# Optimization experiments

Measured on AMD Instinct MI355X. Metric: run time of the kernel, lower is better.

Reference implementation:

```python
import jax, jax.numpy as jnp
import numpy as np
from jax import lax

GAMMA = 0.99
LAM = 0.95
CLIP_PARAM = 0.2
VALUE_LOSS_COEF = 0.5
ENTROPY_COEF = 0.01
EPS = 1e-09

B, T = 4096, 2048


def setup_inputs() -> dict:
    key = jax.random.key(0)
    ks = jax.random.split(key, 6)
    rewards = jax.random.normal(ks[0], (B, T), dtype=jnp.float32)
    values = jax.random.normal(ks[1], (B, T + 1), dtype=jnp.float32)
    ref_probs = jax.random.uniform(ks[2], (B, T), dtype=jnp.float32)
    old_probs = jax.random.uniform(ks[3], (B, T), dtype=jnp.float32)
    curr_probs = jax.random.uniform(ks[4], (B, T), dtype=jnp.float32)
    # episode-continuation masks: mostly 1, occasional 0 (episode boundary)
    masks = (jax.random.uniform(ks[5], (B, T)) > 0.02).astype(jnp.float32)
    return {"rewards": rewards, "values": values, "ref_probs": ref_probs,
            "old_probs": old_probs, "curr_probs": curr_probs, "masks": masks}


def compute_gae(rewards, values, masks, gamma, lam):
    # single fused reverse scan over time; per-step state is (B,)
    def step(carry, xs):
        r, v, v_next, m = xs
        delta = r + gamma * v_next * m - v
        adv = delta + gamma * lam * m * carry
        return adv, adv

    xs = (rewards.T, values[:, :-1].T, values[:, 1:].T, masks.T)  # each (T, B)
    _, advs = lax.scan(step, jnp.zeros(rewards.shape[0], rewards.dtype), xs, reverse=True)
    advantages = advs.T  # (B, T)
    returns = advantages + values[:, :-1]
    return advantages, returns


def reference(rewards, values, ref_probs, old_probs, curr_probs, masks):
    advantages, returns = compute_gae(rewards, values, masks, GAMMA, LAM)
    # torch .std() is unbiased (ddof=1)
    advantages = (advantages - advantages.mean()) / (advantages.std(ddof=1) + EPS)
    ratios = curr_probs / (old_probs + EPS)
    surr1 = ratios * advantages
    surr2 = jnp.clip(ratios, 1.0 - CLIP_PARAM, 1.0 + CLIP_PARAM) * advantages
    ppo_loss = -jnp.minimum(surr1, surr2).mean()
    value_loss = jnp.mean((returns - values[:, :-1]) ** 2)
    entropy_loss = -jnp.mean(curr_probs * jnp.log(curr_probs + EPS))
    total_loss = ppo_loss + VALUE_LOSS_COEF * value_loss + ENTROPY_COEF * entropy_loss
    return (total_loss, ppo_loss, VALUE_LOSS_COEF * value_loss, ENTROPY_COEF * entropy_loss)
```

## Files before the change

kernel.cpp:

```cpp
#include <hip/hip_runtime.h>
#include <math.h>


#define GAMMA     0.99f
#define LAM       0.95f
#define CLIP_LO   0.8f
#define CLIP_HI   1.2f
#define EPSF      1e-9f

constexpr int BB = 4096;
constexpr int TT = 2048;
constexpr long long NN = (long long)BB * TT;
constexpr int GAE_BLOCKS = BB;
constexpr int PPO_BLOCKS = 4096;

struct Stats { float mean; float inv; double sum2; };
static constexpr size_t GAE_PART_OFF = 64;
static constexpr size_t PPO_PART_OFF = GAE_PART_OFF + GAE_BLOCKS * sizeof(float2);
static constexpr size_t ADV_OFF      = PPO_PART_OFF + PPO_BLOCKS * sizeof(float2);

__device__ __forceinline__ unsigned bf16_rne(float x) {
    unsigned u = __float_as_uint(x);
    u += 0x7FFFu + ((u >> 16) & 1u);
    return u >> 16;
}

__global__ __launch_bounds__(512, 4) void gae_kernel(
    const float* __restrict__ rewards,
    const float* __restrict__ values,
    const float* __restrict__ masks,
    uint4* __restrict__ advb,
    float2* __restrict__ partials)
{
    const int tid  = threadIdx.x;
    const int lane = tid & 63;
    const int wave = tid >> 6;
    const int e0   = tid * 4;
    const int r    = blockIdx.x;

    __shared__ float2 wT[8];
    __shared__ float  wr1[8], wr2[8];

    const float* rp = rewards + (size_t)r * TT;
    const float* mp = masks   + (size_t)r * TT;
    const size_t vw  = (size_t)r * (TT + 1);
    const int    ofs = (int)(vw & 3);
    const float4* v4 = (const float4*)(values + (vw & ~(size_t)3));

    float4 R  = *(const float4*)(rp + e0);
    float4 M  = *(const float4*)(mp + e0);
    float4 V0 = v4[tid];
    float4 V1 = v4[tid + 1];

    float ff[8] = {V0.x, V0.y, V0.z, V0.w, V1.x, V1.y, V1.z, V1.w};
    float vv[5];
    if (ofs == 0) {
#pragma unroll
        for (int j = 0; j < 5; ++j) vv[j] = ff[j];
    } else if (ofs == 1) {
#pragma unroll
        for (int j = 0; j < 5; ++j) vv[j] = ff[j + 1];
    } else if (ofs == 2) {
#pragma unroll
        for (int j = 0; j < 5; ++j) vv[j] = ff[j + 2];
    } else {
#pragma unroll
        for (int j = 0; j < 5; ++j) vv[j] = ff[j + 3];
    }

    float rr[4] = {R.x, R.y, R.z, R.w};
    float mm[4] = {M.x, M.y, M.z, M.w};

    float la[4], S[4];
    {
        float d[4], c[4];
#pragma unroll
        for (int j = 0; j < 4; ++j) {
            d[j] = rr[j] + GAMMA * vv[j + 1] * mm[j] - vv[j];
            c[j] = (GAMMA * LAM) * mm[j];
        }
        la[3] = d[3]; S[3] = c[3];
#pragma unroll
        for (int j = 2; j >= 0; --j) {
            la[j] = d[j] + c[j] * la[j + 1];
            S[j]  = c[j] * S[j + 1];
        }
    }

    float A = S[0], Bv = la[0];
#pragma unroll
    for (int d2 = 1; d2 < 64; d2 <<= 1) {
        float A2 = __shfl_down(A, d2, 64), B2 = __shfl_down(Bv, d2, 64);
        if (lane + d2 < 64) { Bv = Bv + A * B2; A = A * A2; }
    }
    if (lane == 0) wT[wave] = make_float2(A, Bv);
    __syncthreads();
    float C = 0.f;
    for (int ww = 7; ww > wave; --ww) C = wT[ww].y + wT[ww].x * C;
    float A1 = __shfl_down(A, 1, 64), B1 = __shfl_down(Bv, 1, 64);
    float car = (lane < 63) ? (B1 + A1 * C) : C;

    float s1 = 0.f, s2 = 0.f;
    unsigned hh[4];
#pragma unroll
    for (int j = 0; j < 4; ++j) {
        float a = la[j] + S[j] * car;
        s1 += a; s2 += a * a;
        hh[j] = bf16_rne(a);
    }
    uint2 pk = {hh[0] | (hh[1] << 16), hh[2] | (hh[3] << 16)};
    ((uint2*)advb)[(size_t)r * 512 + tid] = pk;

#pragma unroll
    for (int off = 32; off > 0; off >>= 1) {
        s1 += __shfl_down(s1, off, 64);
        s2 += __shfl_down(s2, off, 64);
    }
    if (lane == 0) { wr1[wave] = s1; wr2[wave] = s2; }
    __syncthreads();
    if (tid == 0) {
        float t1 = 0.f, t2 = 0.f;
#pragma unroll
        for (int w = 0; w < 8; ++w) { t1 += wr1[w]; t2 += wr2[w]; }
        partials[blockIdx.x] = make_float2(t1, t2);
    }
}

__global__ __launch_bounds__(256) void finalize_stats(
    const float2* __restrict__ gp, Stats* __restrict__ stats)
{
    const int tid = threadIdx.x;
    __shared__ double l1[256], l2[256];
    double s1 = 0.0, s2 = 0.0;
    for (int i = tid; i < GAE_BLOCKS; i += 256) {
        float2 p = gp[i];
        s1 += (double)p.x;
        s2 += (double)p.y;
    }
    l1[tid] = s1; l2[tid] = s2;
    __syncthreads();
    for (int st = 128; st > 0; st >>= 1) {
        if (tid < st) { l1[tid] += l1[tid + st]; l2[tid] += l2[tid + st]; }
        __syncthreads();
    }
    if (tid == 0) {
        double S1 = l1[0], S2 = l2[0];
        double mean = S1 / (double)NN;
        double var  = (S2 - S1 * S1 / (double)NN) / (double)(NN - 1);
        stats->mean = (float)mean;
        stats->inv  = (float)(1.0 / (sqrt(var) + 1e-9));
        stats->sum2 = S2;
    }
}

__global__ __launch_bounds__(256, 8) void ppo_kernel(
    const float* __restrict__ adv_bf16,
    const float* __restrict__ oldp,
    const float* __restrict__ currp,
    const Stats* __restrict__ stats,
    float2* __restrict__ partials)
{
    const float mean = stats->mean;
    const float inv  = stats->inv;
    const int tid = threadIdx.x;
    const int i0  = blockIdx.x * 512 + tid;
    const int i1  = i0 + 256;

    const uint2*  a2 = (const uint2*)adv_bf16;
    const float4* o4 = (const float4*)oldp;
    const float4* c4 = (const float4*)currp;

    uint2  A0 = a2[i0], A1 = a2[i1];
    float4 O0 = o4[i0], O1 = o4[i1];
    float4 C0 = c4[i0], C1 = c4[i1];

    float av[8] = {__uint_as_float(A0.x << 16), __uint_as_float(A0.x & 0xFFFF0000u),
                   __uint_as_float(A0.y << 16), __uint_as_float(A0.y & 0xFFFF0000u),
                   __uint_as_float(A1.x << 16), __uint_as_float(A1.x & 0xFFFF0000u),
                   __uint_as_float(A1.y << 16), __uint_as_float(A1.y & 0xFFFF0000u)};
    float ov[8] = {O0.x, O0.y, O0.z, O0.w, O1.x, O1.y, O1.z, O1.w};
    float cv[8] = {C0.x, C0.y, C0.z, C0.w, C1.x, C1.y, C1.z, C1.w};

    float sm = 0.f, se = 0.f;
#pragma unroll
    for (int j = 0; j < 8; ++j) {
        float an    = (av[j] - mean) * inv;
        float ratio = cv[j] * __builtin_amdgcn_rcpf(ov[j] + EPSF);
        float rc    = fminf(fmaxf(ratio, CLIP_LO), CLIP_HI);
        sm += fminf(ratio * an, rc * an);
        se += cv[j] * __logf(cv[j] + EPSF);
    }

#pragma unroll
    for (int off = 32; off > 0; off >>= 1) {
        sm += __shfl_down(sm, off, 64);
        se += __shfl_down(se, off, 64);
    }
    __shared__ float w1[4], w2[4];
    const int wave = tid >> 6, lane = tid & 63;
    if (lane == 0) { w1[wave] = sm; w2[wave] = se; }
    __syncthreads();
    if (tid == 0) {
        float2 p = {w1[0] + w1[1] + w1[2] + w1[3],
                    w2[0] + w2[1] + w2[2] + w2[3]};
        partials[blockIdx.x] = p;
    }
}

__global__ __launch_bounds__(256) void finalize_out(
    const float2* __restrict__ pp,
    const Stats* __restrict__ stats,
    float* __restrict__ out)
{
    const int tid = threadIdx.x;
    __shared__ double l1[256], l2[256];
    double s1 = 0.0, s2 = 0.0;
    for (int i = tid; i < PPO_BLOCKS; i += 256) {
        float2 p = pp[i];
        s1 += (double)p.x;
        s2 += (double)p.y;
    }
    l1[tid] = s1; l2[tid] = s2;
    __syncthreads();
    for (int st = 128; st > 0; st >>= 1) {
        if (tid < st) { l1[tid] += l1[tid + st]; l2[tid] += l2[tid + st]; }
        __syncthreads();
    }
    if (tid == 0) {
        double invN = 1.0 / (double)NN;
        double vl   = 0.5  * (stats->sum2 * invN);
        double ppo  = -(l1[0] * invN);
        double ent  = -0.01 * (l2[0] * invN);
        out[0] = (float)(ppo + vl + ent);
        out[1] = (float)ppo;
        out[2] = (float)vl;
        out[3] = (float)ent;
    }
}

extern "C" void kernel_launch(void* const* d_in, const int* in_sizes, int n_in,
                              void* d_out, int out_size, void* d_ws, size_t ws_size,
                              hipStream_t stream) {
    const float* rewards = (const float*)d_in[0];
    const float* values  = (const float*)d_in[1];
    const float* oldp    = (const float*)d_in[3];
    const float* currp   = (const float*)d_in[4];
    const float* masks   = (const float*)d_in[5];

    Stats*  stats = (Stats*)d_ws;
    float2* gaep  = (float2*)((char*)d_ws + GAE_PART_OFF);
    float2* ppop  = (float2*)((char*)d_ws + PPO_PART_OFF);
    uint4*  advb  = (uint4*)((char*)d_ws + ADV_OFF);
    float*  out   = (float*)d_out;

    gae_kernel<<<GAE_BLOCKS, 512, 0, stream>>>(rewards, values, masks, advb, gaep);
    finalize_stats<<<1, 256, 0, stream>>>(gaep, stats);
    ppo_kernel<<<PPO_BLOCKS, 256, 0, stream>>>((const float*)advb, oldp, currp, stats, ppop);
    finalize_out<<<1, 256, 0, stream>>>(ppop, stats, out);
}
```

Measured before the change: 207.3 us.

## Fuse GAE, stats and PPO into one cooperative kernel keeping advantages in LDS

Replaces the four launches with one cooperative kernel of 512 blocks. Each block processes 8 rows, keeps the bf16 advantages in shared memory, and uses grid syncs to compute the global mean/std and then the PPO and entropy sums. This removes the global round-trip of the advantage buffer and three kernel launches. The cost is lower parallelism and occupancy (32KB LDS per block, only 512 blocks), plus three grid-wide barriers.

```diff
diff --git a/kernel.cpp b/kernel.cpp
--- a/kernel.cpp
+++ b/kernel.cpp
@@ -1,4 +1,5 @@
 #include <hip/hip_runtime.h>
+#include <hip/hip_cooperative_groups.h>
 #include <math.h>
 
 
@@ -8,16 +9,18 @@
 #define CLIP_HI   1.2f
 #define EPSF      1e-9f
 
+namespace cg = cooperative_groups;
+
 constexpr int BB = 4096;
 constexpr int TT = 2048;
 constexpr long long NN = (long long)BB * TT;
-constexpr int GAE_BLOCKS = BB;
-constexpr int PPO_BLOCKS = 4096;
+constexpr int NBLK = 512;
+constexpr int NTHR = 512;
+constexpr int RPB  = 8;
 
 struct Stats { float mean; float inv; double sum2; };
 static constexpr size_t GAE_PART_OFF = 64;
-static constexpr size_t PPO_PART_OFF = GAE_PART_OFF + GAE_BLOCKS * sizeof(float2);
-static constexpr size_t ADV_OFF      = PPO_PART_OFF + PPO_BLOCKS * sizeof(float2);
+static constexpr size_t PPO_PART_OFF = GAE_PART_OFF + NBLK * sizeof(float2);
 
 __device__ __forceinline__ unsigned bf16_rne(float x) {
     unsigned u = __float_as_uint(x);
@@ -25,170 +28,163 @@
     return u >> 16;
 }
 
-__global__ __launch_bounds__(512, 4) void gae_kernel(
+__global__ __launch_bounds__(NTHR, 4) void fused_kernel(
     const float* __restrict__ rewards,
     const float* __restrict__ values,
     const float* __restrict__ masks,
-    uint4* __restrict__ advb,
-    float2* __restrict__ partials)
+    const float* __restrict__ oldp,
+    const float* __restrict__ currp,
+    Stats* stats, float2* gaep, float2* ppop, float* out)
 {
+    cg::grid_group grid = cg::this_grid();
     const int tid  = threadIdx.x;
     const int lane = tid & 63;
     const int wave = tid >> 6;
     const int e0   = tid * 4;
-    const int r    = blockIdx.x;
-
-    __shared__ float2 wT[8];
-    __shared__ float  wr1[8], wr2[8];
-
-    const float* rp = rewards + (size_t)r * TT;
-    const float* mp = masks   + (size_t)r * TT;
-    const size_t vw  = (size_t)r * (TT + 1);
-    const int    ofs = (int)(vw & 3);
-    const float4* v4 = (const float4*)(values + (vw & ~(size_t)3));
-
-    float4 R  = *(const float4*)(rp + e0);
-    float4 M  = *(const float4*)(mp + e0);
-    float4 V0 = v4[tid];
-    float4 V1 = v4[tid + 1];
-
-    float ff[8] = {V0.x, V0.y, V0.z, V0.w, V1.x, V1.y, V1.z, V1.w};
-    float vv[5];
-    if (ofs == 0) {
-#pragma unroll
-        for (int j = 0; j < 5; ++j) vv[j] = ff[j];
-    } else if (ofs == 1) {
-#pragma unroll
-        for (int j = 0; j < 5; ++j) vv[j] = ff[j + 1];
-    } else if (ofs == 2) {
-#pragma unroll
-        for (int j = 0; j < 5; ++j) vv[j] = ff[j + 2];
-    } else {
-#pragma unroll
-        for (int j = 0; j < 5; ++j) vv[j] = ff[j + 3];
-    }
-
-    float rr[4] = {R.x, R.y, R.z, R.w};
-    float mm[4] = {M.x, M.y, M.z, M.w};
-
-    float la[4], S[4];
-    {
-        float d[4], c[4];
+
+    __shared__ uint2  advs[RPB][NTHR];
+    __shared__ float2 wT[2][8];
+    __shared__ float  wrA[8], wrB[8];
+    __shared__ double dw1[8], dw2[8];
+
+    float s1 = 0.f, s2 = 0.f;
+
+    for (int k = 0; k < RPB; ++k) {
+        const int r = blockIdx.x * RPB + k;
+
+        const float* rp = rewards + (size_t)r * TT;
+        const float* mp = masks   + (size_t)r * TT;
+        const size_t vw  = (size_t)r * (TT + 1);
+        const int    ofs = (int)(vw & 3);
+        const float4* v4 = (const float4*)(values + (vw & ~(size_t)3));
+
+        float4 R  = *(const float4*)(rp + e0);
+        float4 M  = *(const float4*)(mp + e0);
+        float4 V0 = v4[tid];
+        float4 V1 = v4[tid + 1];
+
+        float ff[8] = {V0.x, V0.y, V0.z, V0.w, V1.x, V1.y, V1.z, V1.w};
+        float vv[5];
+        if (ofs == 0) {
+#pragma unroll
+            for (int j = 0; j < 5; ++j) vv[j] = ff[j];
+        } else if (ofs == 1) {
+#pragma unroll
+            for (int j = 0; j < 5; ++j) vv[j] = ff[j + 1];
+        } else if (ofs == 2) {
+#pragma unroll
+            for (int j = 0; j < 5; ++j) vv[j] = ff[j + 2];
+        } else {
+#pragma unroll
+            for (int j = 0; j < 5; ++j) vv[j] = ff[j + 3];
+        }
+
+        float rr[4] = {R.x, R.y, R.z, R.w};
+        float mm[4] = {M.x, M.y, M.z, M.w};
+
+        float la[4], S[4];
+        {
+            float d[4], c[4];
+#pragma unroll
+            for (int j = 0; j < 4; ++j) {
+                d[j] = rr[j] + GAMMA * vv[j + 1] * mm[j] - vv[j];
+                c[j] = (GAMMA * LAM) * mm[j];
+            }
+            la[3] = d[3]; S[3] = c[3];
+#pragma unroll
+            for (int j = 2; j >= 0; --j) {
+                la[j] = d[j] + c[j] * la[j + 1];
+                S[j]  = c[j] * S[j + 1];
+            }
+        }
+
+        float A = S[0], Bv = la[0];
+#pragma unroll
+        for (int d2 = 1; d2 < 64; d2 <<= 1) {
+            float A2 = __shfl_down(A, d2, 64), B2 = __shfl_down(Bv, d2, 64);
+            if (lane + d2 < 64) { Bv = Bv + A * B2; A = A * A2; }
+        }
+        if (lane == 0) wT[k & 1][wave] = make_float2(A, Bv);
+        __syncthreads();
+        float C = 0.f;
+        for (int ww = 7; ww > wave; --ww)
+            C = wT[k & 1][ww].y + wT[k & 1][ww].x * C;
+        float A1 = __shfl_down(A, 1, 64), B1 = __shfl_down(Bv, 1, 64);
+        float car = (lane < 63) ? (B1 + A1 * C) : C;
+
+        unsigned hh[4];
 #pragma unroll
         for (int j = 0; j < 4; ++j) {
-            d[j] = rr[j] + GAMMA * vv[j + 1] * mm[j] - vv[j];
-            c[j] = (GAMMA * LAM) * mm[j];
-        }
-        la[3] = d[3]; S[3] = c[3];
-#pragma unroll
-        for (int j = 2; j >= 0; --j) {
-            la[j] = d[j] + c[j] * la[j + 1];
-            S[j]  = c[j] * S[j + 1];
-        }
-    }
-
-    float A = S[0], Bv = la[0];
-#pragma unroll
-    for (int d2 = 1; d2 < 64; d2 <<= 1) {
-        float A2 = __shfl_down(A, d2, 64), B2 = __shfl_down(Bv, d2, 64);
-        if (lane + d2 < 64) { Bv = Bv + A * B2; A = A * A2; }
-    }
-    if (lane == 0) wT[wave] = make_float2(A, Bv);
-    __syncthreads();
-    float C = 0.f;
-    for (int ww = 7; ww > wave; --ww) C = wT[ww].y + wT[ww].x * C;
-    float A1 = __shfl_down(A, 1, 64), B1 = __shfl_down(Bv, 1, 64);
-    float car = (lane < 63) ? (B1 + A1 * C) : C;
-
-    float s1 = 0.f, s2 = 0.f;
-    unsigned hh[4];
-#pragma unroll
-    for (int j = 0; j < 4; ++j) {
-        float a = la[j] + S[j] * car;
-        s1 += a; s2 += a * a;
-        hh[j] = bf16_rne(a);
-    }
-    uint2 pk = {hh[0] | (hh[1] << 16), hh[2] | (hh[3] << 16)};
-    ((uint2*)advb)[(size_t)r * 512 + tid] = pk;
+            float a = la[j] + S[j] * car;
+            s1 += a; s2 += a * a;
+            hh[j] = bf16_rne(a);
+        }
+        advs[k][tid] = make_uint2(hh[0] | (hh[1] << 16), hh[2] | (hh[3] << 16));
+    }
 
 #pragma unroll
     for (int off = 32; off > 0; off >>= 1) {
         s1 += __shfl_down(s1, off, 64);
         s2 += __shfl_down(s2, off, 64);
     }
-    if (lane == 0) { wr1[wave] = s1; wr2[wave] = s2; }
+    if (lane == 0) { wrA[wave] = s1; wrB[wave] = s2; }
     __syncthreads();
     if (tid == 0) {
         float t1 = 0.f, t2 = 0.f;
 #pragma unroll
-        for (int w = 0; w < 8; ++w) { t1 += wr1[w]; t2 += wr2[w]; }
-        partials[blockIdx.x] = make_float2(t1, t2);
-    }
-}
-
-__global__ __launch_bounds__(256) void finalize_stats(
-    const float2* __restrict__ gp, Stats* __restrict__ stats)
-{
-    const int tid = threadIdx.x;
-    __shared__ double l1[256], l2[256];
-    double s1 = 0.0, s2 = 0.0;
-    for (int i = tid; i < GAE_BLOCKS; i += 256) {
-        float2 p = gp[i];
-        s1 += (double)p.x;
-        s2 += (double)p.y;
-    }
-    l1[tid] = s1; l2[tid] = s2;
-    __syncthreads();
-    for (int st = 128; st > 0; st >>= 1) {
-        if (tid < st) { l1[tid] += l1[tid + st]; l2[tid] += l2[tid + st]; }
+        for (int w = 0; w < 8; ++w) { t1 += wrA[w]; t2 += wrB[w]; }
+        gaep[blockIdx.x] = make_float2(t1, t2);
+    }
+    __threadfence();
+    grid.sync();
+
+    if (blockIdx.x == 0) {
+        float2 p = gaep[tid];
+        double d1 = (double)p.x, d2 = (double)p.y;
+#pragma unroll
+        for (int off = 32; off > 0; off >>= 1) {
+            d1 += __shfl_down(d1, off, 64);
+            d2 += __shfl_down(d2, off, 64);
+        }
+        if (lane == 0) { dw1[wave] = d1; dw2[wave] = d2; }
         __syncthreads();
-    }
-    if (tid == 0) {
-        double S1 = l1[0], S2 = l2[0];
-        double mean = S1 / (double)NN;
-        double var  = (S2 - S1 * S1 / (double)NN) / (double)(NN - 1);
-        stats->mean = (float)mean;
-        stats->inv  = (float)(1.0 / (sqrt(var) + 1e-9));
-        stats->sum2 = S2;
-    }
-}
-
-__global__ __launch_bounds__(256, 8) void ppo_kernel(
-    const float* __restrict__ adv_bf16,
-    const float* __restrict__ oldp,
-    const float* __restrict__ currp,
-    const Stats* __restrict__ stats,
-    float2* __restrict__ partials)
-{
+        if (tid == 0) {
+            double S1 = 0.0, S2 = 0.0;
+#pragma unroll
+            for (int w = 0; w < 8; ++w) { S1 += dw1[w]; S2 += dw2[w]; }
+            double mean = S1 / (double)NN;
+            double var  = (S2 - S1 * S1 / (double)NN) / (double)(NN - 1);
+            stats->mean = (float)mean;
+            stats->inv  = (float)(1.0 / (sqrt(var) + 1e-9));
+            stats->sum2 = S2;
+        }
+        __threadfence();
+    }
+    grid.sync();
+
     const float mean = stats->mean;
     const float inv  = stats->inv;
-    const int tid = threadIdx.x;
-    const int i0  = blockIdx.x * 512 + tid;
-    const int i1  = i0 + 256;
-
-    const uint2*  a2 = (const uint2*)adv_bf16;
     const float4* o4 = (const float4*)oldp;
     const float4* c4 = (const float4*)currp;
 
-    uint2  A0 = a2[i0], A1 = a2[i1];
-    float4 O0 = o4[i0], O1 = o4[i1];
-    float4 C0 = c4[i0], C1 = c4[i1];
-
-    float av[8] = {__uint_as_float(A0.x << 16), __uint_as_float(A0.x & 0xFFFF0000u),
-                   __uint_as_float(A0.y << 16), __uint_as_float(A0.y & 0xFFFF0000u),
-                   __uint_as_float(A1.x << 16), __uint_as_float(A1.x & 0xFFFF0000u),
-                   __uint_as_float(A1.y << 16), __uint_as_float(A1.y & 0xFFFF0000u)};
-    float ov[8] = {O0.x, O0.y, O0.z, O0.w, O1.x, O1.y, O1.z, O1.w};
-    float cv[8] = {C0.x, C0.y, C0.z, C0.w, C1.x, C1.y, C1.z, C1.w};
-
     float sm = 0.f, se = 0.f;
-#pragma unroll
-    for (int j = 0; j < 8; ++j) {
-        float an    = (av[j] - mean) * inv;
-        float ratio = cv[j] * __builtin_amdgcn_rcpf(ov[j] + EPSF);
-        float rc    = fminf(fmaxf(ratio, CLIP_LO), CLIP_HI);
-        sm += fminf(ratio * an, rc * an);
-        se += cv[j] * __logf(cv[j] + EPSF);
+    for (int k = 0; k < RPB; ++k) {
+        const size_t r = (size_t)blockIdx.x * RPB + k;
+        float4 O  = o4[r * 512 + tid];
+        float4 Cc = c4[r * 512 + tid];
+        uint2  A  = advs[k][tid];
+        float av[4] = {__uint_as_float(A.x << 16), __uint_as_float(A.x & 0xFFFF0000u),
+                       __uint_as_float(A.y << 16), __uint_as_float(A.y & 0xFFFF0000u)};
+        float ov[4] = {O.x, O.y, O.z, O.w};
+        float cv[4] = {Cc.x, Cc.y, Cc.z, Cc.w};
+#pragma unroll
+        for (int j = 0; j < 4; ++j) {
+            float an    = (av[j] - mean) * inv;
+            float ratio = cv[j] * __builtin_amdgcn_rcpf(ov[j] + EPSF);
+            float rc    = fminf(fmaxf(ratio, CLIP_LO), CLIP_HI);
+            sm += fminf(ratio * an, rc * an);
+            se += cv[j] * __logf(cv[j] + EPSF);
+        }
     }
 
 #pragma unroll
@@ -196,45 +192,40 @@
         sm += __shfl_down(sm, off, 64);
         se += __shfl_down(se, off, 64);
     }
-    __shared__ float w1[4], w2[4];
-    const int wave = tid >> 6, lane = tid & 63;
-    if (lane == 0) { w1[wave] = sm; w2[wave] = se; }
+    if (lane == 0) { wrA[wave] = sm; wrB[wave] = se; }
     __syncthreads();
     if (tid == 0) {
-        float2 p = {w1[0] + w1[1] + w1[2] + w1[3],
-                    w2[0] + w2[1] + w2[2] + w2[3]};
-        partials[blockIdx.x] = p;
-    }
-}
-
-__global__ __launch_bounds__(256) void finalize_out(
-    const float2* __restrict__ pp,
-    const Stats* __restrict__ stats,
-    float* __restrict__ out)
-{
-    const int tid = threadIdx.x;
-    __shared__ double l1[256], l2[256];
-    double s1 = 0.0, s2 = 0.0;
-    for (int i = tid; i < PPO_BLOCKS; i += 256) {
-        float2 p = pp[i];
-        s1 += (double)p.x;
-        s2 += (double)p.y;
-    }
-    l1[tid] = s1; l2[tid] = s2;
-    __syncthreads();
-    for (int st = 128; st > 0; st >>= 1) {
-        if (tid < st) { l1[tid] += l1[tid + st]; l2[tid] += l2[tid + st]; }
+        float t1 = 0.f, t2 = 0.f;
+#pragma unroll
+        for (int w = 0; w < 8; ++w) { t1 += wrA[w]; t2 += wrB[w]; }
+        ppop[blockIdx.x] = make_float2(t1, t2);
+    }
+    __threadfence();
+    grid.sync();
+
+    if (blockIdx.x == 0) {
+        float2 p = ppop[tid];
+        double d1 = (double)p.x, d2 = (double)p.y;
+#pragma unroll
+        for (int off = 32; off > 0; off >>= 1) {
+            d1 += __shfl_down(d1, off, 64);
+            d2 += __shfl_down(d2, off, 64);
+        }
+        if (lane == 0) { dw1[wave] = d1; dw2[wave] = d2; }
         __syncthreads();
-    }
-    if (tid == 0) {
-        double invN = 1.0 / (double)NN;
-        double vl   = 0.5  * (stats->sum2 * invN);
-        double ppo  = -(l1[0] * invN);
-        double ent  = -0.01 * (l2[0] * invN);
-        out[0] = (float)(ppo + vl + ent);
-        out[1] = (float)ppo;
-        out[2] = (float)vl;
-        out[3] = (float)ent;
+        if (tid == 0) {
+            double Sm = 0.0, Se = 0.0;
+#pragma unroll
+            for (int w = 0; w < 8; ++w) { Sm += dw1[w]; Se += dw2[w]; }
+            double invN = 1.0 / (double)NN;
+            double vl   = 0.5  * (stats->sum2 * invN);
+            double ppo  = -(Sm * invN);
+            double ent  = -0.01 * (Se * invN);
+            out[0] = (float)(ppo + vl + ent);
+            out[1] = (float)ppo;
+            out[2] = (float)vl;
+            out[3] = (float)ent;
+        }
     }
 }
 
@@ -250,11 +241,11 @@
     Stats*  stats = (Stats*)d_ws;
     float2* gaep  = (float2*)((char*)d_ws + GAE_PART_OFF);
     float2* ppop  = (float2*)((char*)d_ws + PPO_PART_OFF);
-    uint4*  advb  = (uint4*)((char*)d_ws + ADV_OFF);
     float*  out   = (float*)d_out;
 
-    gae_kernel<<<GAE_BLOCKS, 512, 0, stream>>>(rewards, values, masks, advb, gaep);
-    finalize_stats<<<1, 256, 0, stream>>>(gaep, stats);
-    ppo_kernel<<<PPO_BLOCKS, 256, 0, stream>>>((const float*)advb, oldp, currp, stats, ppop);
-    finalize_out<<<1, 256, 0, stream>>>(ppop, stats, out);
+    void* args[] = {(void*)&rewards, (void*)&values, (void*)&masks,
+                    (void*)&oldp, (void*)&currp,
+                    (void*)&stats, (void*)&gaep, (void*)&ppop, (void*)&out};
+    hipLaunchCooperativeKernel((const void*)fused_kernel,
+                               dim3(NBLK), dim3(NTHR), args, 0, stream);
 }
```

After: 497.2 us. 140% more time.
